# Kernel tuning notes

Hardware: AMD Instinct MI355X
Metric: run time of the kernel (lower is better)

The kernel has to match this reference:

```python
import math
import jax, jax.numpy as jnp
import numpy as np

VOCAB, D, H, L, DFF, MAXLEN, PAD = 32000, 512, 8, 6, 2048, 5000, 0
DK = D // H
EPS = 1e-5


def _positional_encoding(max_len, d_model):
    pos = np.arange(max_len, dtype=np.float32)[:, None]
    div = np.exp(np.arange(0, d_model, 2, dtype=np.float32) * (-math.log(10000.0) / d_model))
    pe = np.zeros((max_len, d_model), dtype=np.float32)
    pe[:, 0::2] = np.sin(pos * div)
    pe[:, 1::2] = np.cos(pos * div)
    return jnp.asarray(pe)


def setup_inputs() -> dict:
    key = jax.random.key(0)
    ks = jax.random.split(key, 16)
    B, S = 2, 2048
    src = jax.random.randint(ks[0], (B, S), 0, VOCAB)
    emb = jax.random.normal(ks[1], (VOCAB, D), jnp.float32) * (D ** -0.5)
    emb = emb.at[PAD].set(0.0)  # padding_idx row zeroed
    pe = _positional_encoding(MAXLEN, D)
    s = 0.02
    WQ = jax.random.normal(ks[2], (L, D, D), jnp.float32) * s
    WK = jax.random.normal(ks[3], (L, D, D), jnp.float32) * s
    WV = jax.random.normal(ks[4], (L, D, D), jnp.float32) * s
    WO = jax.random.normal(ks[5], (L, D, D), jnp.float32) * s
    W1 = jax.random.normal(ks[6], (L, D, DFF), jnp.float32) * s
    b1 = jnp.zeros((L, DFF), jnp.float32)
    W2 = jax.random.normal(ks[7], (L, DFF, D), jnp.float32) * s
    b2 = jnp.zeros((L, D), jnp.float32)
    ln1_s = jnp.ones((L, D), jnp.float32); ln1_b = jnp.zeros((L, D), jnp.float32)
    ln2_s = jnp.ones((L, D), jnp.float32); ln2_b = jnp.zeros((L, D), jnp.float32)
    fn_s = jnp.ones((D,), jnp.float32); fn_b = jnp.zeros((D,), jnp.float32)
    return dict(src=src, emb=emb, pe=pe, WQ=WQ, WK=WK, WV=WV, WO=WO,
                W1=W1, b1=b1, W2=W2, b2=b2, ln1_s=ln1_s, ln1_b=ln1_b,
                ln2_s=ln2_s, ln2_b=ln2_b, fn_s=fn_s, fn_b=fn_b)


def _layernorm(x, scale, bias):
    mu = jnp.mean(x, axis=-1, keepdims=True)
    var = jnp.mean(jnp.square(x - mu), axis=-1, keepdims=True)
    return (x - mu) * jax.lax.rsqrt(var + EPS) * scale + bias


def _encoder_forward(src, emb, pe, WQ, WK, WV, WO, W1, b1, W2, b2,
                     ln1_s, ln1_b, ln2_s, ln2_b, fn_s, fn_b):
    B, S = src.shape
    key_mask = (src != PAD)[:, None, None, :]  # [B,1,1,S] padding mask
    x = emb[src] * math.sqrt(D) + pe[:S]        # [B,S,D] (dropout=eval/off)
    for l in range(L):
        # --- pre-LN self-attention ---
        h = _layernorm(x, ln1_s[l], ln1_b[l])
        q = (h @ WQ[l]).reshape(B, S, H, DK).transpose(0, 2, 1, 3)
        k = (h @ WK[l]).reshape(B, S, H, DK).transpose(0, 2, 1, 3)
        v = (h @ WV[l]).reshape(B, S, H, DK).transpose(0, 2, 1, 3)
        scores = jnp.einsum('bhqd,bhkd->bhqk', q, k) / math.sqrt(DK)
        scores = jnp.where(key_mask, scores, -jnp.inf)
        w = jax.nn.softmax(scores, axis=-1)
        w = jnp.nan_to_num(w, nan=0.0)
        attn = jnp.einsum('bhqk,bhkd->bhqd', w, v)
        attn = attn.transpose(0, 2, 1, 3).reshape(B, S, D) @ WO[l]
        x = x + attn
        # --- pre-LN FFN ---
        h = _layernorm(x, ln2_s[l], ln2_b[l])
        h = jax.nn.relu(h @ W1[l] + b1[l]) @ W2[l] + b2[l]
        x = x + h
    return _layernorm(x, fn_s, fn_b)


def reference(src, emb, pe, WQ, WK, WV, WO, W1, b1, W2, b2,
              ln1_s, ln1_b, ln2_s, ln2_b, fn_s, fn_b):
    return _encoder_forward(src, emb, pe, WQ, WK, WV, WO, W1, b1, W2, b2,
                            ln1_s, ln1_b, ln2_s, ln2_b, fn_s, fn_b)
```

## Files before the change

### kernel.cpp

```cpp
#include <hip/hip_runtime.h>


typedef _Float16 f16;
typedef _Float16 f16x8 __attribute__((ext_vector_type(8)));
typedef _Float16 f16x4 __attribute__((ext_vector_type(4)));
typedef float    f32x4 __attribute__((ext_vector_type(4)));

#define MFMA16(a, b, c) __builtin_amdgcn_mfma_f32_16x16x32_f16((a), (b), (c), 0, 0, 0)
#define GLOAD_LDS16(GP, LP)                                        \
  __builtin_amdgcn_global_load_lds(                                \
      (const __attribute__((address_space(1))) void*)(GP),         \
      (__attribute__((address_space(3))) void*)(LP), 16, 0, 0)

__device__ inline float fast_exp2(float x) {
#if __has_builtin(__builtin_amdgcn_exp2f)
  return __builtin_amdgcn_exp2f(x);
#else
  return exp2f(x);
#endif
}

static constexpr int Dm  = 512;
static constexpr int Sx  = 2048;
static constexpr int NTOK = 4096;
static constexpr int DFFm = 2048;
static constexpr int Lc  = 6;

__global__ __launch_bounds__(256) void transpose_qkvo(
    const float* __restrict__ WQ, const float* __restrict__ WK,
    const float* __restrict__ WV, const float* __restrict__ WO,
    f16* __restrict__ wqkv, f16* __restrict__ wtO)
{
  __shared__ float t[32][33];
  const int z = blockIdx.z;
  const int widx = z / 6, layer = z % 6;
  const float* src = ((widx == 0) ? WQ : (widx == 1) ? WK : (widx == 2) ? WV : WO)
                     + (size_t)layer * Dm * Dm;
  f16* dst = (widx < 3)
      ? wqkv + (size_t)layer * 1536 * Dm + (size_t)widx * 512 * Dm
      : wtO + (size_t)layer * Dm * Dm;
  const int r0 = blockIdx.y * 32, c0 = blockIdx.x * 32;
  const int tx = threadIdx.x, ty = threadIdx.y;
  #pragma unroll
  for (int i = 0; i < 4; i++)
    t[ty + i * 8][tx] = src[(size_t)(r0 + ty + i * 8) * Dm + c0 + tx];
  __syncthreads();
  #pragma unroll
  for (int i = 0; i < 4; i++)
    dst[(size_t)(c0 + ty + i * 8) * Dm + r0 + tx] = (f16)t[tx][ty + i * 8];
}

__global__ __launch_bounds__(256) void transpose_cvt(
    const float* __restrict__ in, f16* __restrict__ out, int R, int C, size_t zs)
{
  __shared__ float t[32][33];
  const int z = blockIdx.z;
  const float* src = in + (size_t)z * zs;
  f16* dst = out + (size_t)z * zs;
  const int r0 = blockIdx.y * 32, c0 = blockIdx.x * 32;
  const int tx = threadIdx.x, ty = threadIdx.y;
  #pragma unroll
  for (int i = 0; i < 4; i++)
    t[ty + i * 8][tx] = src[(size_t)(r0 + ty + i * 8) * C + c0 + tx];
  __syncthreads();
  #pragma unroll
  for (int i = 0; i < 4; i++)
    dst[(size_t)(c0 + ty + i * 8) * R + r0 + tx] = (f16)t[tx][ty + i * 8];
}

__global__ __launch_bounds__(256) void embed_k(
    const int* __restrict__ src, const float* __restrict__ emb,
    const float* __restrict__ pe, float* __restrict__ x, float* __restrict__ mb)
{
  const int gid = blockIdx.x * 256 + threadIdx.x;
  const int token = gid >> 6;
  const int d0 = (gid & 63) << 3;
  const int s = token & (Sx - 1);
  const int tk = src[token];
  if ((gid & 63) == 0) mb[token] = (tk != 0) ? 0.f : -3.0e38f;
  const float* e = emb + (size_t)tk * Dm + d0;
  const float* p = pe + (size_t)s * Dm + d0;
  float* o = x + (size_t)token * Dm + d0;
  const float SC = 22.627416997969522f;
  #pragma unroll
  for (int j = 0; j < 8; j++) o[j] = e[j] * SC + p[j];
}

template <typename OUT, int ADD, int BIAS, int WRITEX>
__global__ __launch_bounds__(256) void lnf_k(
    const float* __restrict__ x, const f16* __restrict__ part,
    const f16* __restrict__ part2, const float* __restrict__ bias,
    const float* __restrict__ sc, const float* __restrict__ bi,
    OUT* __restrict__ out, float* __restrict__ xout)
{
  const int row = blockIdx.x * 4 + (threadIdx.x >> 6);
  const int l = threadIdx.x & 63;
  const float* px = x + (size_t)row * Dm + l * 8;
  float v[8];
  *(float4*)&v[0] = *(const float4*)px;
  *(float4*)&v[4] = *(const float4*)(px + 4);
  if constexpr (ADD >= 1) {
    f16x8 p = *(const f16x8*)(part + (size_t)row * Dm + l * 8);
    #pragma unroll
    for (int j = 0; j < 8; j++) v[j] += (float)p[j];
    if constexpr (ADD == 2) {
      f16x8 p2 = *(const f16x8*)(part2 + (size_t)row * Dm + l * 8);
      #pragma unroll
      for (int j = 0; j < 8; j++) v[j] += (float)p2[j];
    }
    if constexpr (BIAS) {
      float bb[8];
      *(float4*)&bb[0] = *(const float4*)(bias + l * 8);
      *(float4*)&bb[4] = *(const float4*)(bias + l * 8 + 4);
      #pragma unroll
      for (int j = 0; j < 8; j++) v[j] += bb[j];
    }
    if constexpr (WRITEX) {
      float* pxo = xout + (size_t)row * Dm + l * 8;
      *(float4*)pxo = *(const float4*)&v[0];
      *(float4*)(pxo + 4) = *(const float4*)&v[4];
    }
  }
  float s = 0.f;
  #pragma unroll
  for (int j = 0; j < 8; j++) s += v[j];
  #pragma unroll
  for (int m = 1; m < 64; m <<= 1) s += __shfl_xor(s, m);
  const float mu = s * (1.0f / 512.0f);
  float qv = 0.f;
  #pragma unroll
  for (int j = 0; j < 8; j++) { float d = v[j] - mu; qv += d * d; }
  #pragma unroll
  for (int m = 1; m < 64; m <<= 1) qv += __shfl_xor(qv, m);
  const float inv = rsqrtf(qv * (1.0f / 512.0f) + 1e-5f);
  float scv[8], biv[8];
  *(float4*)&scv[0] = *(const float4*)(sc + l * 8);
  *(float4*)&scv[4] = *(const float4*)(sc + l * 8 + 4);
  *(float4*)&biv[0] = *(const float4*)(bi + l * 8);
  *(float4*)&biv[4] = *(const float4*)(bi + l * 8 + 4);
  if constexpr (sizeof(OUT) == 2) {
    f16x8 o;
    #pragma unroll
    for (int j = 0; j < 8; j++) o[j] = (f16)((v[j] - mu) * inv * scv[j] + biv[j]);
    *(f16x8*)((f16*)out + (size_t)row * Dm + l * 8) = o;
  } else {
    float o[8];
    #pragma unroll
    for (int j = 0; j < 8; j++) o[j] = (v[j] - mu) * inv * scv[j] + biv[j];
    float* po = (float*)out + (size_t)row * Dm + l * 8;
    *(float4*)po = *(float4*)&o[0];
    *(float4*)(po + 4) = *(float4*)&o[4];
  }
}

template <int BN, int MODE, int N, int K, int SK>
__global__ __launch_bounds__(256) void gemm_k(
    const f16* __restrict__ A, const f16* __restrict__ Bt,
    f16* __restrict__ O0, f16* __restrict__ O1, f16* __restrict__ O2,
    const float* __restrict__ bias)
{
  constexpr int BM = 128;
  constexpr int NF = (BN >= 32) ? BN / 32 : 1;
  constexpr int NBM = NTOK / BM;
  constexpr int NBN = N / BN;
  constexpr int NB = NBM * NBN * SK;
  __shared__ f16 lsA[2][BM * 64];
  __shared__ f16 lsB[2][BN * 64];
  const int tid = threadIdx.x;
  const int l = tid & 63, w = tid >> 6;
  const int lr = l & 15, lh = l >> 4;
  const int wm = w >> 1, wn = w & 1;
  const int bid = blockIdx.x;
  const int nid = (bid & 7) * (NB / 8) + (bid >> 3);
  const int ks = nid / (NBM * NBN);
  const int rr = nid % (NBM * NBN);
  const int bm = rr / NBN, bn = rr % NBN;

  constexpr int ACH = (BM * 64) / (256 * 8);
  constexpr int BCH = (BN * 64) / (256 * 8);
  const size_t rowA0 = (size_t)bm * BM;
  const size_t rowB0 = (size_t)bn * BN;
  const int k0 = ks * (K / SK);

  auto stage = [&](int kt, int pb) {
    #pragma unroll
    for (int i = 0; i < ACH; i++) {
      int c = i * 256 + tid, r = c >> 3, g = c & 7, gs = g ^ (r & 7);
      GLOAD_LDS16(A + (rowA0 + r) * K + k0 + kt * 64 + gs * 8, &lsA[pb][c * 8]);
    }
    #pragma unroll
    for (int i = 0; i < BCH; i++) {
      int c = i * 256 + tid, r = c >> 3, g = c & 7, gs = g ^ (r & 7);
      GLOAD_LDS16(Bt + (rowB0 + r) * K + k0 + kt * 64 + gs * 8, &lsB[pb][c * 8]);
    }
  };

  f32x4 acc[4][NF] = {};
  stage(0, 0);
  constexpr int NT = (K / SK) >> 6;
  for (int kt = 0; kt < NT; ++kt) {
    const int cur = kt & 1;
    __syncthreads();
    if (kt + 1 < NT) stage(kt + 1, cur ^ 1);
    #pragma unroll
    for (int s = 0; s < 2; s++) {
      const int gg = (s * 4 + lh) ^ (lr & 7);
      f16x8 af[4], bf[NF];
      #pragma unroll
      for (int mf = 0; mf < 4; mf++)
        af[mf] = *(const f16x8*)(&lsA[cur][(wm * 64 + mf * 16 + lr) * 64 + gg * 8]);
      #pragma unroll
      for (int nf = 0; nf < NF; nf++)
        bf[nf] = *(const f16x8*)(&lsB[cur][(wn * (BN / 2) + nf * 16 + lr) * 64 + gg * 8]);
      #pragma unroll
      for (int mf = 0; mf < 4; mf++)
        #pragma unroll
        for (int nf = 0; nf < NF; nf++)
          acc[mf][nf] = MFMA16(af[mf], bf[nf], acc[mf][nf]);
    }
  }

  #pragma unroll
  for (int mf = 0; mf < 4; mf++) {
    #pragma unroll
    for (int nf = 0; nf < NF; nf++) {
      const int token = bm * BM + wm * 64 + mf * 16 + lh * 4;
      const int ch = bn * BN + wn * (BN / 2) + nf * 16 + lr;
      if constexpr (MODE == 0) {
        const int part = ch >> 9;
        const int pch = ch & 511;
        if (part == 2) {
          f16x4 o;
          #pragma unroll
          for (int r = 0; r < 4; r++) o[r] = (f16)acc[mf][nf][r];
          const int bb = token >> 11, ss = token & (Sx - 1);
          const int scol = (ss & ~31) | (((ss >> 2) & 3) << 3) | (((ss >> 4) & 1) << 2);
          *(f16x4*)(O2 + ((size_t)((bb << 3) + (pch >> 6)) * 64 + (pch & 63)) * Sx + scol) = o;
        } else {
          f16* Oz = (part == 0) ? O0 : O1;
          #pragma unroll
          for (int r = 0; r < 4; r++)
            Oz[(size_t)(token + r) * Dm + pch] = (f16)acc[mf][nf][r];
        }
      } else if constexpr (MODE == 1) {
        #pragma unroll
        for (int r = 0; r < 4; r++)
          O0[(size_t)(token + r) * N + ch] = (f16)acc[mf][nf][r];
      } else if constexpr (MODE == 2) {
        #pragma unroll
        for (int r = 0; r < 4; r++) {
          float v = acc[mf][nf][r] + bias[ch];
          O0[(size_t)(token + r) * N + ch] = (f16)fmaxf(v, 0.f);
        }
      } else {
        f16* dst = O0 + (size_t)ks * NTOK * N;
        #pragma unroll
        for (int r = 0; r < 4; r++)
          dst[(size_t)(token + r) * N + ch] = (f16)acc[mf][nf][r];
      }
    }
  }
}

__global__ __launch_bounds__(512) void attn_k(
    const f16* __restrict__ q, const f16* __restrict__ kk,
    const f16* __restrict__ vt, const float* __restrict__ maskb,
    f16* __restrict__ out)
{
  __shared__ f16 lsK[2][2][64 * 64];
  __shared__ f16 lsV[2][2][64 * 64];
  const int tid = threadIdx.x;
  const int l = tid & 63, w = tid >> 6;
  const int lr = l & 15, lh = l >> 4;
  const int grp = w >> 2;
  const int t256 = tid & 255;
  const int bid = blockIdx.x;
  const int nid = ((bid & 7) << 6) + (bid >> 3);
  const int bh = nid >> 5;
  const int qt = nid & 31;
  const int b = bh >> 3, h = bh & 7;

  const _Float16 QS = (_Float16)0.18033688f;
  f16x8 qf[2];
  #pragma unroll
  for (int s = 0; s < 2; s++) {
    size_t row = (size_t)(b * Sx + qt * 64 + (w & 3) * 16 + lr);
    f16x8 t = *(const f16x8*)(q + row * Dm + h * 64 + s * 32 + lh * 8);
    qf[s] = t * QS;
  }

  const f16x8 ones = {(f16)1, (f16)1, (f16)1, (f16)1,
                      (f16)1, (f16)1, (f16)1, (f16)1};
  f32x4 oacc[4] = {};
  f32x4 sumacc = {};
  float mrun = -1e30f;

  auto stage = [&](int t, int pb) {
    #pragma unroll
    for (int i = 0; i < 2; i++) {
      int c = i * 256 + t256, r = c >> 3, g = c & 7, gs = g ^ (r & 7);
      GLOAD_LDS16(kk + (size_t)(b * Sx + t * 64 + r) * Dm + h * 64 + gs * 8,
                  &lsK[grp][pb][c * 8]);
      GLOAD_LDS16(vt + (size_t)(bh * 64 + r) * Sx + t * 64 + gs * 8,
                  &lsV[grp][pb][c * 8]);
    }
  };
  stage(grp * 16, 0);

  for (int i = 0; i < 16; ++i) {
    const int t = grp * 16 + i;
    const int cur = i & 1;
    __syncthreads();
    if (i < 15) stage(t + 1, cur ^ 1);

    f32x4 sacc[4];
    #pragma unroll
    for (int kf = 0; kf < 4; kf++)
      sacc[kf] = *(const f32x4*)(maskb + b * Sx + t * 64 + kf * 16 + lh * 4);
    __builtin_amdgcn_s_setprio(1);
    #pragma unroll
    for (int s = 0; s < 2; s++) {
      const int gk = (s * 4 + lh) ^ (lr & 7);
      #pragma unroll
      for (int kf = 0; kf < 4; kf++) {
        f16x8 a = *(const f16x8*)(&lsK[grp][cur][(kf * 16 + lr) * 64 + gk * 8]);
        sacc[kf] = MFMA16(a, qf[s], sacc[kf]);
      }
    }
    __builtin_amdgcn_s_setprio(0);

    float pmax;
    {
      float t0 = fmaxf(fmaxf(sacc[0][0], sacc[0][1]), sacc[0][2]);
      float t1 = fmaxf(fmaxf(sacc[0][3], sacc[1][0]), sacc[1][1]);
      float t2 = fmaxf(fmaxf(sacc[1][2], sacc[1][3]), sacc[2][0]);
      float t3 = fmaxf(fmaxf(sacc[2][1], sacc[2][2]), sacc[2][3]);
      float t4 = fmaxf(fmaxf(sacc[3][0], sacc[3][1]), sacc[3][2]);
      float u0 = fmaxf(fmaxf(t0, t1), sacc[3][3]);
      float u1 = fmaxf(fmaxf(t2, t3), t4);
      pmax = fmaxf(u0, u1);
    }
    pmax = fmaxf(pmax, __shfl_xor(pmax, 16));
    pmax = fmaxf(pmax, __shfl_xor(pmax, 32));
    if (!__all(pmax - mrun <= 8.0f)) {
      const float mnew = fmaxf(mrun, pmax);
      const float rs = fast_exp2(mrun - mnew);
      sumacc *= rs;
      #pragma unroll
      for (int mf = 0; mf < 4; mf++) oacc[mf] *= rs;
      mrun = mnew;
    }
    #pragma unroll
    for (int kf = 0; kf < 4; kf++)
      #pragma unroll
      for (int r = 0; r < 4; r++)
        sacc[kf][r] = fast_exp2(sacc[kf][r] - mrun);
    f16x8 pa[2];
    #pragma unroll
    for (int s = 0; s < 2; s++)
      #pragma unroll
      for (int jj = 0; jj < 8; jj++)
        pa[s][jj] = (f16)sacc[2 * s + (jj >> 2)][jj & 3];
    sumacc = MFMA16(ones, pa[0], sumacc);
    sumacc = MFMA16(ones, pa[1], sumacc);

    __builtin_amdgcn_s_setprio(1);
    #pragma unroll
    for (int s = 0; s < 2; s++) {
      const int gv = (4 * s + lh) ^ (lr & 7);
      #pragma unroll
      for (int mf = 0; mf < 4; mf++) {
        f16x8 vv = *(const f16x8*)(&lsV[grp][cur][(mf * 16 + lr) * 64 + gv * 8]);
        oacc[mf] = MFMA16(vv, pa[s], oacc[mf]);
      }
    }
    __builtin_amdgcn_s_setprio(0);
  }

  const float lrun = sumacc[0];
  __syncthreads();
  float* sO  = (float*)&lsK[0][0][0];
  float* sML = (float*)&lsV[0][0][0];
  const int wl = (w & 3) * 64 + l;
  if (grp == 1) {
    #pragma unroll
    for (int mf = 0; mf < 4; mf++)
      #pragma unroll
      for (int r = 0; r < 4; r++) sO[wl * 16 + mf * 4 + r] = oacc[mf][r];
    sML[wl * 2] = mrun;
    sML[wl * 2 + 1] = lrun;
  }
  __syncthreads();
  if (grp == 0) {
    const float m1 = sML[wl * 2], l1 = sML[wl * 2 + 1];
    const float mm = fmaxf(mrun, m1);
    const float s0 = fast_exp2(mrun - mm), s1 = fast_exp2(m1 - mm);
    const float inv = 1.f / (lrun * s0 + l1 * s1);
    size_t row = (size_t)(b * Sx + qt * 64 + (w & 3) * 16 + lr);
    #pragma unroll
    for (int mf = 0; mf < 4; mf++) {
      f16x4 o;
      #pragma unroll
      for (int r = 0; r < 4; r++)
        o[r] = (f16)((oacc[mf][r] * s0 + sO[wl * 16 + mf * 4 + r] * s1) * inv);
      *(f16x4*)(out + row * Dm + h * 64 + mf * 16 + lh * 4) = o;
    }
  }
}

extern "C" void kernel_launch(void* const* d_in, const int* in_sizes, int n_in,
                              void* d_out, int out_size, void* d_ws, size_t ws_size,
                              hipStream_t stream)
{
  (void)in_sizes; (void)n_in; (void)out_size; (void)ws_size;
  const int*   src  = (const int*)d_in[0];
  const float* emb  = (const float*)d_in[1];
  const float* pe   = (const float*)d_in[2];
  const float* WQ   = (const float*)d_in[3];
  const float* WK   = (const float*)d_in[4];
  const float* WV   = (const float*)d_in[5];
  const float* WO   = (const float*)d_in[6];
  const float* W1   = (const float*)d_in[7];
  const float* b1   = (const float*)d_in[8];
  const float* W2   = (const float*)d_in[9];
  const float* b2   = (const float*)d_in[10];
  const float* ln1s = (const float*)d_in[11];
  const float* ln1b = (const float*)d_in[12];
  const float* ln2s = (const float*)d_in[13];
  const float* ln2b = (const float*)d_in[14];
  const float* fns  = (const float*)d_in[15];
  const float* fnb  = (const float*)d_in[16];

  char* ws = (char*)d_ws;
  const size_t DD = (size_t)Dm * Dm;
  const size_t DQKV = (size_t)1536 * Dm;
  const size_t DF = (size_t)Dm * DFFm;
  f16* wqkv = (f16*)(ws);
  f16* wtO  = wqkv + Lc * DQKV;
  f16* wt1  = wtO + Lc * DD;
  f16* wt2  = wt1 + Lc * DF;
  float* x  = (float*)(wt2 + Lc * DF);
  f16* hbuf = (f16*)(x + (size_t)NTOK * Dm);
  f16* qb   = hbuf + (size_t)NTOK * Dm;
  f16* kb   = qb + (size_t)NTOK * Dm;
  f16* vtb  = kb + (size_t)NTOK * Dm;
  f16* attn = vtb + (size_t)NTOK * Dm;
  f16* aout = attn + (size_t)NTOK * Dm;
  f16* ff   = aout + (size_t)NTOK * Dm;
  f16* ffo  = ff + (size_t)NTOK * DFFm;
  float* maskb = (float*)(ffo + (size_t)2 * NTOK * Dm);

  const dim3 tb(32, 8);
  transpose_qkvo<<<dim3(16, 16, 24), tb, 0, stream>>>(WQ, WK, WV, WO, wqkv, wtO);
  transpose_cvt<<<dim3(64, 16, Lc), tb, 0, stream>>>(W1, wt1, Dm, DFFm, DF);
  transpose_cvt<<<dim3(16, 64, Lc), tb, 0, stream>>>(W2, wt2, DFFm, Dm, DF);

  embed_k<<<1024, 256, 0, stream>>>(src, emb, pe, x, maskb);

  f16* ffo1 = ffo + (size_t)NTOK * Dm;
  for (int l = 0; l < Lc; l++) {
    const f16* wqkv_l = wqkv + (size_t)l * DQKV;
    const f16* wo = wtO + (size_t)l * DD;
    const f16* w1 = wt1 + (size_t)l * DF;
    const f16* w2 = wt2 + (size_t)l * DF;

    if (l == 0)
      lnf_k<f16, 0, 0, 0><<<1024, 256, 0, stream>>>(
          x, nullptr, nullptr, nullptr, ln1s, ln1b, hbuf, nullptr);
    else
      lnf_k<f16, 2, 1, 1><<<1024, 256, 0, stream>>>(
          x, ffo, ffo1, b2 + (size_t)(l - 1) * Dm, ln1s + l * Dm, ln1b + l * Dm,
          hbuf, x);
    gemm_k<64, 0, 1536, 512, 1><<<768, 256, 0, stream>>>(
        hbuf, wqkv_l, qb, kb, vtb, nullptr);
    attn_k<<<512, 512, 0, stream>>>(qb, kb, vtb, maskb, attn);
    gemm_k<32, 1, 512, 512, 1><<<512, 256, 0, stream>>>(
        attn, wo, aout, nullptr, nullptr, nullptr);
    lnf_k<f16, 1, 0, 1><<<1024, 256, 0, stream>>>(
        x, aout, nullptr, nullptr, ln2s + l * Dm, ln2b + l * Dm, hbuf, x);
    gemm_k<128, 2, 2048, 512, 1><<<512, 256, 0, stream>>>(
        hbuf, w1, ff, nullptr, nullptr, b1 + (size_t)l * DFFm);
    gemm_k<64, 3, 512, 2048, 2><<<512, 256, 0, stream>>>(
        ff, w2, ffo, nullptr, nullptr, nullptr);
  }

  lnf_k<float, 2, 1, 0><<<1024, 256, 0, stream>>>(
      x, ffo, ffo1, b2 + (size_t)(Lc - 1) * Dm, fns, fnb, (float*)d_out, x);
}
```

Baseline: 623.6 us.

## Store residual stream in fp16 and merge weight transposes into one launch

The residual activation x, read and written by the embedding and every layernorm kernel, changes from fp32 to fp16, which halves the memory traffic of those bandwidth-bound kernels. The three weight transpose/convert launches are also merged into a single flat-grid kernel to cut launch overhead. The fp16 residual accumulates rounding error across six layers and can overflow or lose precision, which risks accuracy.

```diff
diff --git a/kernel.cpp b/kernel.cpp
--- a/kernel.cpp
+++ b/kernel.cpp
@@ -26,38 +26,44 @@
 static constexpr int DFFm = 2048;
 static constexpr int Lc  = 6;
 
-__global__ __launch_bounds__(256) void transpose_qkvo(
+__global__ __launch_bounds__(256) void transpose_all(
     const float* __restrict__ WQ, const float* __restrict__ WK,
     const float* __restrict__ WV, const float* __restrict__ WO,
-    f16* __restrict__ wqkv, f16* __restrict__ wtO)
+    const float* __restrict__ W1, const float* __restrict__ W2,
+    f16* __restrict__ wqkv, f16* __restrict__ wtO,
+    f16* __restrict__ wt1, f16* __restrict__ wt2)
 {
   __shared__ float t[32][33];
-  const int z = blockIdx.z;
-  const int widx = z / 6, layer = z % 6;
-  const float* src = ((widx == 0) ? WQ : (widx == 1) ? WK : (widx == 2) ? WV : WO)
-                     + (size_t)layer * Dm * Dm;
-  f16* dst = (widx < 3)
-      ? wqkv + (size_t)layer * 1536 * Dm + (size_t)widx * 512 * Dm
-      : wtO + (size_t)layer * Dm * Dm;
-  const int r0 = blockIdx.y * 32, c0 = blockIdx.x * 32;
-  const int tx = threadIdx.x, ty = threadIdx.y;
-  #pragma unroll
-  for (int i = 0; i < 4; i++)
-    t[ty + i * 8][tx] = src[(size_t)(r0 + ty + i * 8) * Dm + c0 + tx];
-  __syncthreads();
-  #pragma unroll
-  for (int i = 0; i < 4; i++)
-    dst[(size_t)(c0 + ty + i * 8) * Dm + r0 + tx] = (f16)t[tx][ty + i * 8];
-}
-
-__global__ __launch_bounds__(256) void transpose_cvt(
-    const float* __restrict__ in, f16* __restrict__ out, int R, int C, size_t zs)
-{
-  __shared__ float t[32][33];
-  const int z = blockIdx.z;
-  const float* src = in + (size_t)z * zs;
-  f16* dst = out + (size_t)z * zs;
-  const int r0 = blockIdx.y * 32, c0 = blockIdx.x * 32;
+  const size_t DD = (size_t)Dm * Dm;
+  const size_t DQKV = (size_t)1536 * Dm;
+  const size_t DF = (size_t)Dm * DFFm;
+  int id = blockIdx.x;
+  const float* src; f16* dst; int R, C, bx, by;
+  if (id < 6144) {
+    const int z = id >> 8, rem = id & 255;
+    bx = rem & 15; by = rem >> 4;
+    const int widx = z / 6, layer = z % 6;
+    src = ((widx == 0) ? WQ : (widx == 1) ? WK : (widx == 2) ? WV : WO)
+          + (size_t)layer * DD;
+    dst = (widx < 3) ? wqkv + (size_t)layer * DQKV + (size_t)widx * 512 * Dm
+                     : wtO + (size_t)layer * DD;
+    R = 512; C = 512;
+  } else if (id < 12288) {
+    id -= 6144;
+    const int layer = id >> 10, rem = id & 1023;
+    bx = rem & 63; by = rem >> 6;
+    src = W1 + (size_t)layer * DF;
+    dst = wt1 + (size_t)layer * DF;
+    R = 512; C = 2048;
+  } else {
+    id -= 12288;
+    const int layer = id >> 10, rem = id & 1023;
+    bx = rem & 15; by = rem >> 4;
+    src = W2 + (size_t)layer * DF;
+    dst = wt2 + (size_t)layer * DF;
+    R = 2048; C = 512;
+  }
+  const int r0 = by * 32, c0 = bx * 32;
   const int tx = threadIdx.x, ty = threadIdx.y;
   #pragma unroll
   for (int i = 0; i < 4; i++)
@@ -70,7 +76,7 @@
 
 __global__ __launch_bounds__(256) void embed_k(
     const int* __restrict__ src, const float* __restrict__ emb,
-    const float* __restrict__ pe, float* __restrict__ x, float* __restrict__ mb)
+    const float* __restrict__ pe, f16* __restrict__ x, float* __restrict__ mb)
 {
   const int gid = blockIdx.x * 256 + threadIdx.x;
   const int token = gid >> 6;
@@ -80,25 +86,26 @@
   if ((gid & 63) == 0) mb[token] = (tk != 0) ? 0.f : -3.0e38f;
   const float* e = emb + (size_t)tk * Dm + d0;
   const float* p = pe + (size_t)s * Dm + d0;
-  float* o = x + (size_t)token * Dm + d0;
   const float SC = 22.627416997969522f;
-  #pragma unroll
-  for (int j = 0; j < 8; j++) o[j] = e[j] * SC + p[j];
+  f16x8 o;
+  #pragma unroll
+  for (int j = 0; j < 8; j++) o[j] = (f16)(e[j] * SC + p[j]);
+  *(f16x8*)(x + (size_t)token * Dm + d0) = o;
 }
 
 template <typename OUT, int ADD, int BIAS, int WRITEX>
 __global__ __launch_bounds__(256) void lnf_k(
-    const float* __restrict__ x, const f16* __restrict__ part,
+    const f16* __restrict__ x, const f16* __restrict__ part,
     const f16* __restrict__ part2, const float* __restrict__ bias,
     const float* __restrict__ sc, const float* __restrict__ bi,
-    OUT* __restrict__ out, float* __restrict__ xout)
+    OUT* __restrict__ out, f16* __restrict__ xout)
 {
   const int row = blockIdx.x * 4 + (threadIdx.x >> 6);
   const int l = threadIdx.x & 63;
-  const float* px = x + (size_t)row * Dm + l * 8;
+  f16x8 xv = *(const f16x8*)(x + (size_t)row * Dm + l * 8);
   float v[8];
-  *(float4*)&v[0] = *(const float4*)px;
-  *(float4*)&v[4] = *(const float4*)(px + 4);
+  #pragma unroll
+  for (int j = 0; j < 8; j++) v[j] = (float)xv[j];
   if constexpr (ADD >= 1) {
     f16x8 p = *(const f16x8*)(part + (size_t)row * Dm + l * 8);
     #pragma unroll
@@ -116,9 +123,10 @@
       for (int j = 0; j < 8; j++) v[j] += bb[j];
     }
     if constexpr (WRITEX) {
-      float* pxo = xout + (size_t)row * Dm + l * 8;
-      *(float4*)pxo = *(const float4*)&v[0];
-      *(float4*)(pxo + 4) = *(const float4*)&v[4];
+      f16x8 xo;
+      #pragma unroll
+      for (int j = 0; j < 8; j++) xo[j] = (f16)v[j];
+      *(f16x8*)(xout + (size_t)row * Dm + l * 8) = xo;
     }
   }
   float s = 0.f;
@@ -439,8 +447,8 @@
   f16* wtO  = wqkv + Lc * DQKV;
   f16* wt1  = wtO + Lc * DD;
   f16* wt2  = wt1 + Lc * DF;
-  float* x  = (float*)(wt2 + Lc * DF);
-  f16* hbuf = (f16*)(x + (size_t)NTOK * Dm);
+  f16* x    = wt2 + Lc * DF;
+  f16* hbuf = x + (size_t)NTOK * Dm;
   f16* qb   = hbuf + (size_t)NTOK * Dm;
   f16* kb   = qb + (size_t)NTOK * Dm;
   f16* vtb  = kb + (size_t)NTOK * Dm;
@@ -450,11 +458,8 @@
   f16* ffo  = ff + (size_t)NTOK * DFFm;
   float* maskb = (float*)(ffo + (size_t)2 * NTOK * Dm);
 
-  const dim3 tb(32, 8);
-  transpose_qkvo<<<dim3(16, 16, 24), tb, 0, stream>>>(WQ, WK, WV, WO, wqkv, wtO);
-  transpose_cvt<<<dim3(64, 16, Lc), tb, 0, stream>>>(W1, wt1, Dm, DFFm, DF);
-  transpose_cvt<<<dim3(16, 64, Lc), tb, 0, stream>>>(W2, wt2, DFFm, Dm, DF);
-
+  transpose_all<<<18432, dim3(32, 8), 0, stream>>>(
+      WQ, WK, WV, WO, W1, W2, wqkv, wtO, wt1, wt2);
   embed_k<<<1024, 256, 0, stream>>>(src, emb, pe, x, maskb);
 
   f16* ffo1 = ffo + (size_t)NTOK * Dm;
@@ -485,5 +490,5 @@
   }
 
   lnf_k<float, 2, 1, 0><<<1024, 256, 0, stream>>>(
-      x, ffo, ffo1, b2 + (size_t)(Lc - 1) * Dm, fns, fnb, (float*)d_out, x);
-}
+      x, ffo, ffo1, b2 + (size_t)(Lc - 1) * Dm, fns, fnb, (float*)d_out, nullptr);
+}
```

Result: faster. 600.1 us (-3.8%).
